# Kernel tuning notes

Measured on AMD Instinct MI355X. Metric: run time of the kernel, lower is better.

Reference implementation:

```python
import jax, jax.numpy as jnp
import numpy as np

B, CTX = 16, 64
H, W = 1024, 1024
EPS = 1e-12
STD = 0.001


def setup_inputs() -> dict:
    key = jax.random.key(0)
    ks = jax.random.split(key, 6)
    x = jax.random.normal(ks[0], (B, CTX), dtype=jnp.float32)
    # context_transform_input / gate: Linear(CTX -> 12) with bias
    lim = 1.0 / np.sqrt(CTX)
    W_in = jax.random.uniform(ks[1], (12, CTX), jnp.float32, -lim, lim)
    b_in = jax.random.uniform(ks[2], (12,), jnp.float32, -lim, lim)
    W_gate = jax.random.uniform(ks[3], (12, CTX), jnp.float32, -lim, lim)
    b_gate = jax.random.uniform(ks[4], (12,), jnp.float32, -lim, lim)
    # base weights: [1, 2, 2, H, W, 2], normal(0, STD)
    weights = STD * jax.random.normal(ks[5], (1, 2, 2, H, W, 2), dtype=jnp.float32)
    return {"x": x, "W_in": W_in, "b_in": b_in, "W_gate": W_gate,
            "b_gate": b_gate, "weights": weights}


def _clerp(z1, z2, c):
    # complex lerp: z1 + c*(z2 - z1) with complex c packed in last dim
    c0, c1 = c[..., 0], c[..., 1]
    re = (1 - c0) * z1[..., 0] + c0 * z2[..., 0] - c1 * (z2[..., 1] - z1[..., 1])
    im = (1 - c0) * z1[..., 1] + c0 * z2[..., 1] + c1 * (z2[..., 0] - z1[..., 0])
    return jnp.stack([re, im], axis=-1)


def _caddmul(z1, z2, bias):
    # bias + z1*z2 (complex), packed in last dim
    re = bias[..., 0] + (z1[..., 0] * z2[..., 0] - z1[..., 1] * z2[..., 1])
    im = bias[..., 1] + (z1[..., 0] * z2[..., 1] + z1[..., 1] * z2[..., 0])
    return jnp.stack([re, im], axis=-1)


def reference(x, W_in, b_in, W_gate, b_gate, weights):
    b = x.shape[0]
    x_t = x @ W_in.T + b_in          # [B, 12]
    x_g = x @ W_gate.T + b_gate      # [B, 12]
    mod = (x_t * jnp.tanh(x_g)).reshape(b, 3, 2, 1, 1, 2)  # broadcasts over H, W
    shift_lerp = jnp.array([0.5, 0.0], dtype=x.dtype)
    shift_scale = jnp.array([1.0, 0.0], dtype=x.dtype)
    param_l = mod[:, 0] + shift_lerp   # [B, 2, 1, 1, 2]
    param_b = mod[:, 1]
    param_s = mod[:, 2] + shift_scale
    w0, w1 = weights[:, 0], weights[:, 1]   # [1, 2, H, W, 2] each
    z = _clerp(w0, w1, param_l)             # [B, 2, H, W, 2]
    z = _caddmul(z, param_s, param_b)       # [B, 2, H, W, 2]
    denom = jnp.sqrt(jnp.sum(z[:, 1] ** 2, axis=-1) + EPS)[..., None]  # [B, H, W, 1]
    theta = z[:, 1] / denom
    return jnp.sum(z[:, 0] * theta, axis=-1)  # [B, H, W]
```

## Files before the change

### kernel.cpp

```cpp
#include <hip/hip_runtime.h>
#include <math.h>

#define HW (1024*1024)
#define BATCH 16

__global__ __launch_bounds__(192) void params_kernel(
    const float* __restrict__ x,
    const float* __restrict__ W_in,
    const float* __restrict__ b_in,
    const float* __restrict__ W_gate,
    const float* __restrict__ b_gate,
    float* __restrict__ par)
{
    __shared__ float smod[BATCH][12];
    int t = threadIdx.x;
    int b = t / 12, j = t % 12;
    {
        const float4* x4  = (const float4*)(x + b * 64);
        const float4* wi4 = (const float4*)(W_in + j * 64);
        const float4* wg4 = (const float4*)(W_gate + j * 64);
        float xt = b_in[j], xg = b_gate[j];
#pragma unroll
        for (int k = 0; k < 16; ++k) {
            float4 xv = x4[k], wi = wi4[k], wg = wg4[k];
            xt = fmaf(xv.x, wi.x, xt); xg = fmaf(xv.x, wg.x, xg);
            xt = fmaf(xv.y, wi.y, xt); xg = fmaf(xv.y, wg.y, xg);
            xt = fmaf(xv.z, wi.z, xt); xg = fmaf(xv.z, wg.z, xg);
            xt = fmaf(xv.w, wi.w, xt); xg = fmaf(xv.w, wg.w, xg);
        }
        smod[b][j] = xt * tanhf(xg);
    }
    __syncthreads();
    if (t < 32) {
        int bb = t >> 1, c = t & 1;
        float l0 = smod[bb][0 + c * 2 + 0] + 0.5f;
        float l1 = smod[bb][0 + c * 2 + 1];
        float br = smod[bb][4 + c * 2 + 0];
        float bi = smod[bb][4 + c * 2 + 1];
        float s0 = smod[bb][8 + c * 2 + 0] + 1.0f;
        float s1 = smod[bb][8 + c * 2 + 1];
        float omr = 1.0f - l0, omi = -l1;
        float Ar = s0 * omr - s1 * omi;
        float Ai = s0 * omi + s1 * omr;
        float Br = s0 * l0 - s1 * l1;
        float Bi = s0 * l1 + s1 * l0;
        float* p = par + (bb * 2 + c) * 6;
        p[0] = Ar; p[1] = Ai; p[2] = Br; p[3] = Bi; p[4] = br; p[5] = bi;
    }
}

__global__ __launch_bounds__(256) void main_kernel(
    const float* __restrict__ wts,
    const float* __restrict__ par,
    float* __restrict__ out)
{
    const int t = threadIdx.x;
    const int idx = blockIdx.x * 256 + t;
    const float4* w4 = (const float4*)wts;

    float4 Wv[4][2];
#pragma unroll
    for (int jc = 0; jc < 4; ++jc) {
        Wv[jc][0] = w4[jc * (HW / 2) + idx * 2 + 0];
        Wv[jc][1] = w4[jc * (HW / 2) + idx * 2 + 1];
    }
    const float* w00 = (const float*)Wv[0];
    const float* w01 = (const float*)Wv[1];
    const float* w10 = (const float*)Wv[2];
    const float* w11 = (const float*)Wv[3];

    float4* out4 = (float4*)out;
#pragma unroll
    for (int b = 0; b < BATCH; ++b) {
        const float* p0 = par + (b * 2 + 0) * 6;
        const float* p1 = par + (b * 2 + 1) * 6;
        float A0r = p0[0], A0i = p0[1], B0r = p0[2], B0i = p0[3], c0r = p0[4], c0i = p0[5];
        float A1r = p1[0], A1i = p1[1], B1r = p1[2], B1i = p1[3], c1r = p1[4], c1i = p1[5];

        float4 o;
        float* op = (float*)&o;
#pragma unroll
        for (int p = 0; p < 4; ++p) {
            float a0r = w00[p * 2], a0i = w00[p * 2 + 1];
            float b0r = w10[p * 2], b0i = w10[p * 2 + 1];
            float a1r = w01[p * 2], a1i = w01[p * 2 + 1];
            float b1r = w11[p * 2], b1i = w11[p * 2 + 1];
            float z0r = c0r + A0r * a0r - A0i * a0i + B0r * b0r - B0i * b0i;
            float z0i = c0i + A0r * a0i + A0i * a0r + B0r * b0i + B0i * b0r;
            float z1r = c1r + A1r * a1r - A1i * a1i + B1r * b1r - B1i * b1i;
            float z1i = c1i + A1r * a1i + A1i * a1r + B1r * b1i + B1i * b1r;
            float rs = rsqrtf(z1r * z1r + z1i * z1i + 1e-12f);
            op[p] = (z0r * z1r + z0i * z1i) * rs;
        }
        out4[b * (HW / 4) + idx] = o;
    }
}

extern "C" void kernel_launch(void* const* d_in, const int* in_sizes, int n_in,
                              void* d_out, int out_size, void* d_ws, size_t ws_size,
                              hipStream_t stream) {
    const float* x      = (const float*)d_in[0];
    const float* W_in   = (const float*)d_in[1];
    const float* b_in   = (const float*)d_in[2];
    const float* W_gate = (const float*)d_in[3];
    const float* b_gate = (const float*)d_in[4];
    const float* wts    = (const float*)d_in[5];
    float* out = (float*)d_out;
    float* par = (float*)d_ws;

    params_kernel<<<1, 192, 0, stream>>>(x, W_in, b_in, W_gate, b_gate, par);
    main_kernel<<<1024, 256, 0, stream>>>(wts, par, out);
}
```

Baseline: 28.55 us.

## Split per-thread work into two float4 halves and defer second weight load

Each thread now handles two disjoint pixel-pair chunks, i0 and i0 + HW/4. It loads one float4 per weight component for the first chunk, computes 8 batches, then issues the second chunk's loads behind a sched_barrier so they overlap with the remaining compute. Output stores become float2 instead of float4. The goal is lower register pressure and better load/compute overlap, at the cost of narrower stores and a changed access layout.

Measured after the change: 31.81 us. 11.4% more time.

```diff
diff --git a/kernel.cpp b/kernel.cpp
--- a/kernel.cpp
+++ b/kernel.cpp
@@ -49,51 +49,61 @@
     }
 }
 
+__device__ __forceinline__ void do_batches(
+    const float4* __restrict__ W, const float* __restrict__ par,
+    float2* __restrict__ out2, int idx, int b0, int b1)
+{
+#pragma unroll
+    for (int b = b0; b < b1; ++b) {
+        const float* p0 = par + (b * 2 + 0) * 6;
+        const float* p1 = par + (b * 2 + 1) * 6;
+        float A0r = p0[0], A0i = p0[1], B0r = p0[2], B0i = p0[3], c0r = p0[4], c0i = p0[5];
+        float A1r = p1[0], A1i = p1[1], B1r = p1[2], B1i = p1[3], c1r = p1[4], c1i = p1[5];
+        float2 o;
+        {
+            float z0r = c0r + A0r * W[0].x - A0i * W[0].y + B0r * W[2].x - B0i * W[2].y;
+            float z0i = c0i + A0r * W[0].y + A0i * W[0].x + B0r * W[2].y + B0i * W[2].x;
+            float z1r = c1r + A1r * W[1].x - A1i * W[1].y + B1r * W[3].x - B1i * W[3].y;
+            float z1i = c1i + A1r * W[1].y + A1i * W[1].x + B1r * W[3].y + B1i * W[3].x;
+            float rs = rsqrtf(z1r * z1r + z1i * z1i + 1e-12f);
+            o.x = (z0r * z1r + z0i * z1i) * rs;
+        }
+        {
+            float z0r = c0r + A0r * W[0].z - A0i * W[0].w + B0r * W[2].z - B0i * W[2].w;
+            float z0i = c0i + A0r * W[0].w + A0i * W[0].z + B0r * W[2].w + B0i * W[2].z;
+            float z1r = c1r + A1r * W[1].z - A1i * W[1].w + B1r * W[3].z - B1i * W[3].w;
+            float z1i = c1i + A1r * W[1].w + A1i * W[1].z + B1r * W[3].w + B1i * W[3].z;
+            float rs = rsqrtf(z1r * z1r + z1i * z1i + 1e-12f);
+            o.y = (z0r * z1r + z0i * z1i) * rs;
+        }
+        out2[b * (HW / 2) + idx] = o;
+    }
+}
+
 __global__ __launch_bounds__(256) void main_kernel(
     const float* __restrict__ wts,
     const float* __restrict__ par,
     float* __restrict__ out)
 {
     const int t = threadIdx.x;
-    const int idx = blockIdx.x * 256 + t;
+    const int i0 = blockIdx.x * 256 + t;
+    const int i1 = i0 + (HW / 4);
     const float4* w4 = (const float4*)wts;
+    float2* out2 = (float2*)out;
 
-    float4 Wv[4][2];
+    float4 WA[4];
 #pragma unroll
-    for (int jc = 0; jc < 4; ++jc) {
-        Wv[jc][0] = w4[jc * (HW / 2) + idx * 2 + 0];
-        Wv[jc][1] = w4[jc * (HW / 2) + idx * 2 + 1];
-    }
-    const float* w00 = (const float*)Wv[0];
-    const float* w01 = (const float*)Wv[1];
-    const float* w10 = (const float*)Wv[2];
-    const float* w11 = (const float*)Wv[3];
+    for (int jc = 0; jc < 4; ++jc) WA[jc] = w4[jc * (HW / 2) + i0];
 
-    float4* out4 = (float4*)out;
+    do_batches(WA, par, out2, i0, 0, 8);
+
+    __builtin_amdgcn_sched_barrier(0);
+    float4 WB[4];
 #pragma unroll
-    for (int b = 0; b < BATCH; ++b) {
-        const float* p0 = par + (b * 2 + 0) * 6;
-        const float* p1 = par + (b * 2 + 1) * 6;
-        float A0r = p0[0], A0i = p0[1], B0r = p0[2], B0i = p0[3], c0r = p0[4], c0i = p0[5];
-        float A1r = p1[0], A1i = p1[1], B1r = p1[2], B1i = p1[3], c1r = p1[4], c1i = p1[5];
+    for (int jc = 0; jc < 4; ++jc) WB[jc] = w4[jc * (HW / 2) + i1];
 
-        float4 o;
-        float* op = (float*)&o;
-#pragma unroll
-        for (int p = 0; p < 4; ++p) {
-            float a0r = w00[p * 2], a0i = w00[p * 2 + 1];
-            float b0r = w10[p * 2], b0i = w10[p * 2 + 1];
-            float a1r = w01[p * 2], a1i = w01[p * 2 + 1];
-            float b1r = w11[p * 2], b1i = w11[p * 2 + 1];
-            float z0r = c0r + A0r * a0r - A0i * a0i + B0r * b0r - B0i * b0i;
-            float z0i = c0i + A0r * a0i + A0i * a0r + B0r * b0i + B0i * b0r;
-            float z1r = c1r + A1r * a1r - A1i * a1i + B1r * b1r - B1i * b1i;
-            float z1i = c1i + A1r * a1i + A1i * a1r + B1r * b1i + B1i * b1r;
-            float rs = rsqrtf(z1r * z1r + z1i * z1i + 1e-12f);
-            op[p] = (z0r * z1r + z0i * z1i) * rs;
-        }
-        out4[b * (HW / 4) + idx] = o;
-    }
+    do_batches(WA, par, out2, i0, 8, 16);
+    do_batches(WB, par, out2, i1, 0, 16);
 }
 
 extern "C" void kernel_launch(void* const* d_in, const int* in_sizes, int n_in,
```
